# Optimization experiments

Hardware: AMD Instinct MI355X
Metric: run time of the kernel (lower is better)

The kernel has to match this reference:

```python
import jax, jax.numpy as jnp
import numpy as np

# db4 analysis filters (pywt.Wavelet('db4').dec_lo / dec_hi)
_DEC_LO = np.array([-0.010597401784997278, 0.032883011666982945, 0.030841381835986965,
                    -0.18703481171888114, -0.02798376941698385, 0.6308807679295904,
                    0.7148465705525415, 0.23037781330885523], dtype=np.float32)
_DEC_HI = np.array([-0.23037781330885523, 0.7148465705525415, -0.6308807679295904,
                    -0.02798376941698385, 0.18703481171888114, 0.030841381835986965,
                    -0.032883011666982945, -0.010597401784997278], dtype=np.float32)
# pytorch_wavelets stores filters reversed (torch conv = correlation); lax.conv is
# also correlation, so use the same reversed filters. Shape [2, 1, L].
_H = jnp.asarray(np.stack([_DEC_LO[::-1], _DEC_HI[::-1]])[:, None, :])

B, SW, SWS, HW, K, J = 2048, 4, 64, 8, 128, 3
DWT_LEN = 84  # 14 (lo, level 3) + 35 (hi1) + 21 (hi2) + 14 (hi3)


def _dwt_level(x, h):
    """One analysis level, mode='reflect' (pytorch_wavelets afb1d). x: [M, N]."""
    N = x.shape[-1]
    L = h.shape[-1]
    outsize = (N + L - 1) // 2          # pywt.dwt_coeff_len, non-periodization
    p = 2 * (outsize - 1) - N + L
    if p % 2 == 1:                       # odd total pad: one extra zero at the end
        x = jnp.pad(x, ((0, 0), (0, 1)))
    x = jnp.pad(x, ((0, 0), (p // 2, p // 2)), mode='reflect')
    y = jax.lax.conv_general_dilated(x[:, None, :], h, (2,), 'VALID')  # [M, 2, out]
    return y[:, 0, :], y[:, 1, :]


def setup_inputs() -> dict:
    key = jax.random.key(0)
    k1, k2, k3 = jax.random.split(key, 3)
    x = jax.random.normal(k1, (B, 1, SW * SWS, HW, HW), dtype=jnp.float32)
    # one Conv3d(1 -> K, kernel=(DWT_LEN, 8, 8)) per subwindow, kaiming-ish init
    fan_in = DWT_LEN * HW * HW
    conv_weight = jax.random.normal(k2, (SW, K, DWT_LEN, HW, HW), dtype=jnp.float32) / np.sqrt(fan_in)
    conv_bias = jax.random.normal(k3, (SW, K), dtype=jnp.float32) * 0.01
    return {"x": x, "conv_weight": conv_weight, "conv_bias": conv_bias}


def reference(x, conv_weight, conv_bias):
    b = x.shape[0]
    # [B,1,T,8,8] -> [B,SW,8,8,SWS]: DWT runs along the time axis of each subwindow
    xt = x[:, 0].reshape(b, SW, SWS, HW, HW).transpose(0, 1, 3, 4, 2)
    xm = xt.reshape(-1, SWS)  # [B*SW*64, 64]
    lo, highs = xm, []
    for _ in range(J):
        lo, hi = _dwt_level(lo, _H)
        highs.append(hi)
    coeffs = jnp.concatenate([lo] + highs, axis=-1)  # [M, 84], order: lo, hi1, hi2, hi3
    c = coeffs.reshape(b, SW, HW, HW, DWT_LEN).transpose(0, 1, 4, 2, 3)  # [B,SW,84,8,8]
    # per-subwindow Conv3d that fully reduces (t,h,w) -> [B, SW, K]
    feat = jnp.einsum('bsthw,skthw->bsk', c, conv_weight) + conv_bias[None]
    # Dropout3d is identity in eval; LeakyReLU default slope 0.01 (typo in source
    # means leakyrelu_negative_slope is never applied)
    return jax.nn.leaky_relu(feat, 0.01).reshape(b, SW * K)
```

## Files before the change

kernel.cpp:

```cpp
#include <hip/hip_runtime.h>
#include <stdint.h>

typedef unsigned int  u32;
typedef unsigned short u16;
typedef __bf16 bf16x8 __attribute__((ext_vector_type(8)));
typedef float  f32x4  __attribute__((ext_vector_type(4)));

__constant__ float GL[8] = { 0.23037781330885523f,  0.7148465705525415f,
                             0.6308807679295904f,  -0.02798376941698385f,
                            -0.18703481171888114f,  0.030841381835986965f,
                             0.032883011666982945f,-0.010597401784997278f };
__constant__ float GH[8] = {-0.010597401784997278f,-0.032883011666982945f,
                             0.030841381835986965f, 0.18703481171888114f,
                            -0.02798376941698385f, -0.6308807679295904f,
                             0.7148465705525415f,  -0.23037781330885523f };

__global__ void build_wdwt(float* __restrict__ Wd) {
    const int j = threadIdx.x;
    float lo1[35], lo2[21];
#pragma unroll
    for (int i = 0; i < 35; ++i) {
        float sl = 0.f, sh = 0.f;
#pragma unroll
        for (int t = 0; t < 8; ++t) {
            int s = 2 * i + t - 6;
            if (s < 0) s = -s;
            if (s >= 64) s = 126 - s;
            float xv = (s == j) ? 1.0f : 0.0f;
            sl += xv * GL[t]; sh += xv * GH[t];
        }
        lo1[i] = sl;
        Wd[(14 + i) * 64 + j] = sh;
    }
#pragma unroll
    for (int i = 0; i < 21; ++i) {
        float sl = 0.f, sh = 0.f;
#pragma unroll
        for (int t = 0; t < 8; ++t) {
            int s = 2 * i + t - 6;
            if (s < 0) s = -s;
            if (s >= 36) s = 70 - s;
            float xv = (s >= 35) ? 0.0f : lo1[s];
            sl += xv * GL[t]; sh += xv * GH[t];
        }
        lo2[i] = sl;
        Wd[(49 + i) * 64 + j] = sh;
    }
#pragma unroll
    for (int i = 0; i < 14; ++i) {
        float sl = 0.f, sh = 0.f;
#pragma unroll
        for (int t = 0; t < 8; ++t) {
            int s = 2 * i + t - 6;
            if (s < 0) s = -s;
            if (s >= 22) s = 42 - s;
            float xv = (s >= 21) ? 0.0f : lo2[s];
            sl += xv * GL[t]; sh += xv * GH[t];
        }
        Wd[i * 64 + j] = sl;
        Wd[(70 + i) * 64 + j] = sh;
    }
}

__device__ inline u16 f32_bf16(float f) {
    u32 u = __float_as_uint(f);
    u += 0x7fffu + ((u >> 16) & 1u);
    return (u16)(u >> 16);
}
__device__ inline u32 pack2_bf16(float a, float b) {
    u32 ua = __float_as_uint(a); ua += 0x7fffu + ((ua >> 16) & 1u);
    u32 ub = __float_as_uint(b); ub += 0x7fffu + ((ub >> 16) & 1u);
    return (ua >> 16) | (ub & 0xffff0000u);
}

__global__ __launch_bounds__(256) void fold_w(const float* __restrict__ cw,
                                              const float* __restrict__ Wd,
                                              u16* __restrict__ Wp) {
    const int sk = blockIdx.x;
    const int hw = threadIdx.x & 63;
    const int tg = __builtin_amdgcn_readfirstlane((int)(threadIdx.x >> 6));
    const int t0 = tg * 16;
    const float* wk = cw + (size_t)sk * (84 * 64);
    float acc[16];
#pragma unroll
    for (int j = 0; j < 16; ++j) acc[j] = 0.f;
#pragma unroll 4
    for (int t = 0; t < 84; ++t) {
        float wv = wk[t * 64 + hw];
        const float* Wr = Wd + t * 64 + t0;
#pragma unroll
        for (int j = 0; j < 16; ++j) acc[j] += wv * Wr[j];
    }
    u16* dst = Wp + (size_t)sk * 4096 + hw;
#pragma unroll
    for (int j = 0; j < 16; ++j) dst[(t0 + j) * 64] = f32_bf16(acc[j]);
}

__global__ __launch_bounds__(256) void gemm_dwt(const float* __restrict__ X,
                                                const u16* __restrict__ Wp,
                                                const float* __restrict__ bias,
                                                float* __restrict__ out) {
    const int nh = blockIdx.x;
    const int mt = blockIdx.y;
    const int s  = blockIdx.z;
    const int tid  = threadIdx.x;
    const int lane = tid & 63;
    const int wv   = tid >> 6;
    const int wm   = wv & 1;
    const int wn   = wv >> 1;
    const int fr   = lane & 15;
    const int fq   = lane >> 4;

    __shared__ __align__(16) u16 Xl[64 * 64];
    __shared__ __align__(16) u16 Wl[64 * 64];

    const int srow = tid >> 2;
    const int sc2  = (tid & 3) * 2;
    const float* xg = X + (size_t)(mt * 64 + srow) * 16384 + s * 4096 + sc2 * 8;
    const u16*   wg = Wp + (size_t)(s * 128 + nh * 64 + srow) * 4096 + sc2 * 8;
    const int xw0 = srow * 64 + (((sc2    ) ^ (srow & 7)) << 3);
    const int xw1 = srow * 64 + (((sc2 + 1) ^ (srow & 7)) << 3);

    const int ar0 = (wm * 32 + fr) * 64;
    const int ar1 = ar0 + 16 * 64;
    const int br0 = (wn * 32 + fr) * 64;
    const int br1 = br0 + 16 * 64;
    const int sk7 = fr & 7;

    f32x4 acc00 = {0.f, 0.f, 0.f, 0.f}, acc01 = acc00, acc10 = acc00, acc11 = acc00;

    float4 xa, xb, xc, xd; uint4 wa, wb;
    {
        const float4* xp = reinterpret_cast<const float4*>(xg);
        xa = xp[0]; xb = xp[1]; xc = xp[2]; xd = xp[3];
        const uint4* wp4 = reinterpret_cast<const uint4*>(wg);
        wa = wp4[0]; wb = wp4[1];
    }

    for (int kt = 0; kt < 64; ++kt) {
        __syncthreads();
        {
            uint4 pa, pb;
            pa.x = pack2_bf16(xa.x, xa.y); pa.y = pack2_bf16(xa.z, xa.w);
            pa.z = pack2_bf16(xb.x, xb.y); pa.w = pack2_bf16(xb.z, xb.w);
            pb.x = pack2_bf16(xc.x, xc.y); pb.y = pack2_bf16(xc.z, xc.w);
            pb.z = pack2_bf16(xd.x, xd.y); pb.w = pack2_bf16(xd.z, xd.w);
            *reinterpret_cast<uint4*>(&Xl[xw0]) = pa;
            *reinterpret_cast<uint4*>(&Xl[xw1]) = pb;
            *reinterpret_cast<uint4*>(&Wl[xw0]) = wa;
            *reinterpret_cast<uint4*>(&Wl[xw1]) = wb;
        }
        __syncthreads();
        {
            const int kn = (kt + 1 < 64) ? kt + 1 : 63;
            const float4* xp = reinterpret_cast<const float4*>(xg + (size_t)kn * 64);
            xa = xp[0]; xb = xp[1]; xc = xp[2]; xd = xp[3];
            const uint4* wp4 = reinterpret_cast<const uint4*>(wg + (size_t)kn * 64);
            wa = wp4[0]; wb = wp4[1];
        }
#pragma unroll
        for (int h = 0; h < 2; ++h) {
            const int q = h * 4 + fq;
            const int co = ((q ^ sk7) << 3);
            bf16x8 a0 = *reinterpret_cast<const bf16x8*>(&Xl[ar0 + co]);
            bf16x8 a1 = *reinterpret_cast<const bf16x8*>(&Xl[ar1 + co]);
            bf16x8 b0 = *reinterpret_cast<const bf16x8*>(&Wl[br0 + co]);
            bf16x8 b1 = *reinterpret_cast<const bf16x8*>(&Wl[br1 + co]);
            acc00 = __builtin_amdgcn_mfma_f32_16x16x32_bf16(a0, b0, acc00, 0, 0, 0);
            acc01 = __builtin_amdgcn_mfma_f32_16x16x32_bf16(a0, b1, acc01, 0, 0, 0);
            acc10 = __builtin_amdgcn_mfma_f32_16x16x32_bf16(a1, b0, acc10, 0, 0, 0);
            acc11 = __builtin_amdgcn_mfma_f32_16x16x32_bf16(a1, b1, acc11, 0, 0, 0);
        }
    }

    const float* bb = bias + s * 128 + nh * 64 + wn * 32;
    float* og = out + (size_t)(mt * 64 + wm * 32) * 512 + s * 128 + nh * 64 + wn * 32;
    const float b0v = bb[fr], b1v = bb[16 + fr];
#pragma unroll
    for (int r = 0; r < 4; ++r) {
        const int row0 = fq * 4 + r;
        float v;
        v = acc00[r] + b0v; og[(size_t)(row0     ) * 512 + fr     ] = v > 0.f ? v : 0.01f * v;
        v = acc01[r] + b1v; og[(size_t)(row0     ) * 512 + 16 + fr] = v > 0.f ? v : 0.01f * v;
        v = acc10[r] + b0v; og[(size_t)(row0 + 16) * 512 + fr     ] = v > 0.f ? v : 0.01f * v;
        v = acc11[r] + b1v; og[(size_t)(row0 + 16) * 512 + 16 + fr] = v > 0.f ? v : 0.01f * v;
    }
}

extern "C" void kernel_launch(void* const* d_in, const int* in_sizes, int n_in,
                              void* d_out, int out_size, void* d_ws, size_t ws_size,
                              hipStream_t stream) {
    const float* x  = (const float*)d_in[0];
    const float* cw = (const float*)d_in[1];
    const float* cb = (const float*)d_in[2];
    float* out = (float*)d_out;

    float* Wd = (float*)d_ws;
    u16*   Wp = (u16*)((char*)d_ws + 32768);

    build_wdwt<<<1, 64, 0, stream>>>(Wd);
    fold_w<<<512, 256, 0, stream>>>(cw, Wd, Wp);
    gemm_dwt<<<dim3(2, 32, 4), 256, 0, stream>>>(x, Wp, cb, out);
}
```

Before: 256.4 us.

## Shrink GEMM M-tile to 16 rows for more blocks; fuse DWT matrix build into fold

The GEMM tile changes from 64x64 to 16x64, so each wave computes one 16x16 MFMA tile. The grid grows fourfold (1024 blocks), which spreads the memory-bound GEMM across more CUs. The single-block build_wdwt kernel is removed: every fold_w block now rebuilds the DWT matrix in shared memory, saving one launch and its serialization. The cost is redundant DWT-matrix work in each of 512 blocks, and each W tile is reloaded four times as often across blocks.

```diff
diff --git a/kernel.cpp b/kernel.cpp
--- a/kernel.cpp
+++ b/kernel.cpp
@@ -15,53 +15,6 @@
                             -0.02798376941698385f, -0.6308807679295904f,
                              0.7148465705525415f,  -0.23037781330885523f };
 
-__global__ void build_wdwt(float* __restrict__ Wd) {
-    const int j = threadIdx.x;
-    float lo1[35], lo2[21];
-#pragma unroll
-    for (int i = 0; i < 35; ++i) {
-        float sl = 0.f, sh = 0.f;
-#pragma unroll
-        for (int t = 0; t < 8; ++t) {
-            int s = 2 * i + t - 6;
-            if (s < 0) s = -s;
-            if (s >= 64) s = 126 - s;
-            float xv = (s == j) ? 1.0f : 0.0f;
-            sl += xv * GL[t]; sh += xv * GH[t];
-        }
-        lo1[i] = sl;
-        Wd[(14 + i) * 64 + j] = sh;
-    }
-#pragma unroll
-    for (int i = 0; i < 21; ++i) {
-        float sl = 0.f, sh = 0.f;
-#pragma unroll
-        for (int t = 0; t < 8; ++t) {
-            int s = 2 * i + t - 6;
-            if (s < 0) s = -s;
-            if (s >= 36) s = 70 - s;
-            float xv = (s >= 35) ? 0.0f : lo1[s];
-            sl += xv * GL[t]; sh += xv * GH[t];
-        }
-        lo2[i] = sl;
-        Wd[(49 + i) * 64 + j] = sh;
-    }
-#pragma unroll
-    for (int i = 0; i < 14; ++i) {
-        float sl = 0.f, sh = 0.f;
-#pragma unroll
-        for (int t = 0; t < 8; ++t) {
-            int s = 2 * i + t - 6;
-            if (s < 0) s = -s;
-            if (s >= 22) s = 42 - s;
-            float xv = (s >= 21) ? 0.0f : lo2[s];
-            sl += xv * GL[t]; sh += xv * GH[t];
-        }
-        Wd[i * 64 + j] = sl;
-        Wd[(70 + i) * 64 + j] = sh;
-    }
-}
-
 __device__ inline u16 f32_bf16(float f) {
     u32 u = __float_as_uint(f);
     u += 0x7fffu + ((u >> 16) & 1u);
@@ -74,11 +27,61 @@
 }
 
 __global__ __launch_bounds__(256) void fold_w(const float* __restrict__ cw,
-                                              const float* __restrict__ Wd,
                                               u16* __restrict__ Wp) {
+    __shared__ float WdL[84 * 64];
+    const int tid = threadIdx.x;
+
+    if (tid < 64) {
+        const int j = tid;
+        float lo1[35], lo2[21];
+#pragma unroll
+        for (int i = 0; i < 35; ++i) {
+            float sl = 0.f, sh = 0.f;
+#pragma unroll
+            for (int t = 0; t < 8; ++t) {
+                int s = 2 * i + t - 6;
+                if (s < 0) s = -s;
+                if (s >= 64) s = 126 - s;
+                float xv = (s == j) ? 1.0f : 0.0f;
+                sl += xv * GL[t]; sh += xv * GH[t];
+            }
+            lo1[i] = sl;
+            WdL[(14 + i) * 64 + j] = sh;
+        }
+#pragma unroll
+        for (int i = 0; i < 21; ++i) {
+            float sl = 0.f, sh = 0.f;
+#pragma unroll
+            for (int t = 0; t < 8; ++t) {
+                int s = 2 * i + t - 6;
+                if (s < 0) s = -s;
+                if (s >= 36) s = 70 - s;
+                float xv = (s >= 35) ? 0.0f : lo1[s];
+                sl += xv * GL[t]; sh += xv * GH[t];
+            }
+            lo2[i] = sl;
+            WdL[(49 + i) * 64 + j] = sh;
+        }
+#pragma unroll
+        for (int i = 0; i < 14; ++i) {
+            float sl = 0.f, sh = 0.f;
+#pragma unroll
+            for (int t = 0; t < 8; ++t) {
+                int s = 2 * i + t - 6;
+                if (s < 0) s = -s;
+                if (s >= 22) s = 42 - s;
+                float xv = (s >= 21) ? 0.0f : lo2[s];
+                sl += xv * GL[t]; sh += xv * GH[t];
+            }
+            WdL[i * 64 + j] = sl;
+            WdL[(70 + i) * 64 + j] = sh;
+        }
+    }
+    __syncthreads();
+
     const int sk = blockIdx.x;
-    const int hw = threadIdx.x & 63;
-    const int tg = __builtin_amdgcn_readfirstlane((int)(threadIdx.x >> 6));
+    const int hw = tid & 63;
+    const int tg = __builtin_amdgcn_readfirstlane((int)(tid >> 6));
     const int t0 = tg * 16;
     const float* wk = cw + (size_t)sk * (84 * 64);
     float acc[16];
@@ -87,7 +90,7 @@
 #pragma unroll 4
     for (int t = 0; t < 84; ++t) {
         float wv = wk[t * 64 + hw];
-        const float* Wr = Wd + t * 64 + t0;
+        const float* Wr = WdL + t * 64 + t0;
 #pragma unroll
         for (int j = 0; j < 16; ++j) acc[j] += wv * Wr[j];
     }
@@ -105,85 +108,79 @@
     const int s  = blockIdx.z;
     const int tid  = threadIdx.x;
     const int lane = tid & 63;
-    const int wv   = tid >> 6;
-    const int wm   = wv & 1;
-    const int wn   = wv >> 1;
+    const int w    = tid >> 6;
     const int fr   = lane & 15;
-    const int fq   = lane >> 4;
+    const int fq   = (lane >> 4) & 3;
 
-    __shared__ __align__(16) u16 Xl[64 * 64];
+    __shared__ __align__(16) u16 Xl[16 * 64];
     __shared__ __align__(16) u16 Wl[64 * 64];
 
-    const int srow = tid >> 2;
-    const int sc2  = (tid & 3) * 2;
-    const float* xg = X + (size_t)(mt * 64 + srow) * 16384 + s * 4096 + sc2 * 8;
-    const u16*   wg = Wp + (size_t)(s * 128 + nh * 64 + srow) * 4096 + sc2 * 8;
-    const int xw0 = srow * 64 + (((sc2    ) ^ (srow & 7)) << 3);
-    const int xw1 = srow * 64 + (((sc2 + 1) ^ (srow & 7)) << 3);
+    const int wrow = tid >> 2;
+    const int wc2  = (tid & 3) * 2;
+    const u16* wg = Wp + (size_t)(s * 128 + nh * 64 + wrow) * 4096 + wc2 * 8;
+    const int ww0 = wrow * 64 + (((wc2    ) ^ (wrow & 7)) << 3);
+    const int ww1 = wrow * 64 + (((wc2 + 1) ^ (wrow & 7)) << 3);
 
-    const int ar0 = (wm * 32 + fr) * 64;
-    const int ar1 = ar0 + 16 * 64;
-    const int br0 = (wn * 32 + fr) * 64;
-    const int br1 = br0 + 16 * 64;
+    const bool doX = tid < 128;
+    const int xrow = (tid >> 3) & 15;
+    const int xch  = tid & 7;
+    const float* xg = X + (size_t)(mt * 16 + xrow) * 16384 + s * 4096 + xch * 8;
+    const int xw = xrow * 64 + ((xch ^ (xrow & 7)) << 3);
+
     const int sk7 = fr & 7;
+    const int ar  = fr * 64;
+    const int br  = (w * 16 + fr) * 64;
 
-    f32x4 acc00 = {0.f, 0.f, 0.f, 0.f}, acc01 = acc00, acc10 = acc00, acc11 = acc00;
+    f32x4 acc = {0.f, 0.f, 0.f, 0.f};
 
-    float4 xa, xb, xc, xd; uint4 wa, wb;
+    float4 xa, xb; uint4 wa, wb;
     {
-        const float4* xp = reinterpret_cast<const float4*>(xg);
-        xa = xp[0]; xb = xp[1]; xc = xp[2]; xd = xp[3];
         const uint4* wp4 = reinterpret_cast<const uint4*>(wg);
         wa = wp4[0]; wb = wp4[1];
+        if (doX) {
+            const float4* xp = reinterpret_cast<const float4*>(xg);
+            xa = xp[0]; xb = xp[1];
+        }
     }
 
     for (int kt = 0; kt < 64; ++kt) {
         __syncthreads();
-        {
-            uint4 pa, pb;
-            pa.x = pack2_bf16(xa.x, xa.y); pa.y = pack2_bf16(xa.z, xa.w);
-            pa.z = pack2_bf16(xb.x, xb.y); pa.w = pack2_bf16(xb.z, xb.w);
-            pb.x = pack2_bf16(xc.x, xc.y); pb.y = pack2_bf16(xc.z, xc.w);
-            pb.z = pack2_bf16(xd.x, xd.y); pb.w = pack2_bf16(xd.z, xd.w);
-            *reinterpret_cast<uint4*>(&Xl[xw0]) = pa;
-            *reinterpret_cast<uint4*>(&Xl[xw1]) = pb;
-            *reinterpret_cast<uint4*>(&Wl[xw0]) = wa;
-            *reinterpret_cast<uint4*>(&Wl[xw1]) = wb;
+        if (doX) {
+            uint4 p;
+            p.x = pack2_bf16(xa.x, xa.y); p.y = pack2_bf16(xa.z, xa.w);
+            p.z = pack2_bf16(xb.x, xb.y); p.w = pack2_bf16(xb.z, xb.w);
+            *reinterpret_cast<uint4*>(&Xl[xw]) = p;
         }
+        *reinterpret_cast<uint4*>(&Wl[ww0]) = wa;
+        *reinterpret_cast<uint4*>(&Wl[ww1]) = wb;
         __syncthreads();
         {
             const int kn = (kt + 1 < 64) ? kt + 1 : 63;
-            const float4* xp = reinterpret_cast<const float4*>(xg + (size_t)kn * 64);
-            xa = xp[0]; xb = xp[1]; xc = xp[2]; xd = xp[3];
             const uint4* wp4 = reinterpret_cast<const uint4*>(wg + (size_t)kn * 64);
             wa = wp4[0]; wb = wp4[1];
+            if (doX) {
+                const float4* xp = reinterpret_cast<const float4*>(xg + (size_t)kn * 64);
+                xa = xp[0]; xb = xp[1];
+            }
         }
 #pragma unroll
         for (int h = 0; h < 2; ++h) {
-            const int q = h * 4 + fq;
+            const int q  = h * 4 + fq;
             const int co = ((q ^ sk7) << 3);
-            bf16x8 a0 = *reinterpret_cast<const bf16x8*>(&Xl[ar0 + co]);
-            bf16x8 a1 = *reinterpret_cast<const bf16x8*>(&Xl[ar1 + co]);
-            bf16x8 b0 = *reinterpret_cast<const bf16x8*>(&Wl[br0 + co]);
-            bf16x8 b1 = *reinterpret_cast<const bf16x8*>(&Wl[br1 + co]);
-            acc00 = __builtin_amdgcn_mfma_f32_16x16x32_bf16(a0, b0, acc00, 0, 0, 0);
-            acc01 = __builtin_amdgcn_mfma_f32_16x16x32_bf16(a0, b1, acc01, 0, 0, 0);
-            acc10 = __builtin_amdgcn_mfma_f32_16x16x32_bf16(a1, b0, acc10, 0, 0, 0);
-            acc11 = __builtin_amdgcn_mfma_f32_16x16x32_bf16(a1, b1, acc11, 0, 0, 0);
+            bf16x8 a = *reinterpret_cast<const bf16x8*>(&Xl[ar + co]);
+            bf16x8 b = *reinterpret_cast<const bf16x8*>(&Wl[br + co]);
+            acc = __builtin_amdgcn_mfma_f32_16x16x32_bf16(a, b, acc, 0, 0, 0);
         }
     }
 
-    const float* bb = bias + s * 128 + nh * 64 + wn * 32;
-    float* og = out + (size_t)(mt * 64 + wm * 32) * 512 + s * 128 + nh * 64 + wn * 32;
-    const float b0v = bb[fr], b1v = bb[16 + fr];
+    const int colg = s * 128 + nh * 64 + w * 16 + fr;
+    const float bv = bias[colg];
+    float* og = out + (size_t)(mt * 16) * 512 + colg;
 #pragma unroll
     for (int r = 0; r < 4; ++r) {
-        const int row0 = fq * 4 + r;
-        float v;
-        v = acc00[r] + b0v; og[(size_t)(row0     ) * 512 + fr     ] = v > 0.f ? v : 0.01f * v;
-        v = acc01[r] + b1v; og[(size_t)(row0     ) * 512 + 16 + fr] = v > 0.f ? v : 0.01f * v;
-        v = acc10[r] + b0v; og[(size_t)(row0 + 16) * 512 + fr     ] = v > 0.f ? v : 0.01f * v;
-        v = acc11[r] + b1v; og[(size_t)(row0 + 16) * 512 + 16 + fr] = v > 0.f ? v : 0.01f * v;
+        const int row = fq * 4 + r;
+        float v = acc[r] + bv;
+        og[(size_t)row * 512] = v > 0.f ? v : 0.01f * v;
     }
 }
 
@@ -195,10 +192,8 @@
     const float* cb = (const float*)d_in[2];
     float* out = (float*)d_out;
 
-    float* Wd = (float*)d_ws;
-    u16*   Wp = (u16*)((char*)d_ws + 32768);
+    u16* Wp = (u16*)d_ws;
 
-    build_wdwt<<<1, 64, 0, stream>>>(Wd);
-    fold_w<<<512, 256, 0, stream>>>(cw, Wd, Wp);
-    gemm_dwt<<<dim3(2, 32, 4), 256, 0, stream>>>(x, Wp, cb, out);
+    fold_w<<<512, 256, 0, stream>>>(cw, Wp);
+    gemm_dwt<<<dim3(2, 128, 4), 256, 0, stream>>>(x, Wp, cb, out);
 }
```

New measurement: 251.7 us. No clear change (-1.8%).
